# Performance work log

Hardware: AMD Instinct MI355X
Metric: run time of the kernel (lower is better)

The kernel has to match this reference:

```python
import jax, jax.numpy as jnp
import numpy as np

N = 20000    # nodes (spots)
E = 320000   # edges per graph (~16 avg degree)
IN = 256     # input feature dim per omics
H = 128      # hidden dim (n_hidden)
L = 3        # layers_nums


def _sage_gcn(src, dst, x, W, b):
    # DGL SAGEConv 'gcn': h_i = (sum_{j in N(i)} x_j + x_i) / (deg_i + 1); out = h @ W + b
    msg = jax.ops.segment_sum(x[src], dst, num_segments=N)
    deg = jax.ops.segment_sum(jnp.ones((src.shape[0],), x.dtype), dst, num_segments=N)
    h = (msg + x) / (deg[:, None] + 1.0)
    return h @ W + b


def _encoder(src, dst, x, W0, b0, Ws, bs):
    h = _sage_gcn(src, dst, x, W0, b0)
    hs = [h]
    for i in range(L - 1):  # dropout=0, res=True (not 'res_add') -> plain stack
        h = _sage_gcn(src, dst, h, Ws[i], bs[i])
        hs.append(h)
    return jnp.stack(hs)  # [L, N, H]


def _decoder(src, dst, x, W0, b0, Ws, bs):
    h = _sage_gcn(src, dst, x, W0, b0)
    for i in range(L - 1):
        h = _sage_gcn(src, dst, h, Ws[i], bs[i])
    return h


def _combine(hstack, wt):
    # propagation_layer_combination with from_logits=True
    w = jax.nn.softmax(wt)
    return jnp.einsum('l,lnh->nh', w, hstack), w


def _attn(e1, e2, w_omega, u_omega):
    emb = jnp.stack([e1, e2], axis=1)          # [N, 2, H]
    v = jnp.tanh(emb @ w_omega)                # [N, 2, H]
    vu = (v @ u_omega)[..., 0]                 # [N, 2]
    alpha = jax.nn.softmax(vu + 1e-6, axis=-1)
    return jnp.einsum('nmh,nm->nh', emb, alpha), alpha


def setup_inputs():
    key = jax.random.key(0)
    ks = iter(jax.random.split(key, 48))

    def ei():
        return jax.random.randint(next(ks), (E,), 0, N, dtype=jnp.int32)

    def w(shape):
        return jax.random.normal(next(ks), shape, jnp.float32) * 0.05

    d = {}
    for g in ['e1s', 'e1f', 'e2s', 'e2f']:
        d[g + '_src'] = ei()
        d[g + '_dst'] = ei()
    d['feat1'] = jax.random.normal(next(ks), (N, IN), jnp.float32)
    d['feat2'] = jax.random.normal(next(ks), (N, IN), jnp.float32)
    for p in ['enc1', 'enc2']:
        d[p + '_W0'] = w((IN, H)); d[p + '_b0'] = jnp.zeros((H,), jnp.float32)
        d[p + '_W'] = w((L - 1, H, H)); d[p + '_b'] = jnp.zeros((L - 1, H), jnp.float32)
    for p in ['dec1', 'dec2']:
        d[p + '_W0'] = w((H, IN)); d[p + '_b0'] = jnp.zeros((IN,), jnp.float32)
        d[p + '_W'] = w((L - 1, IN, IN)); d[p + '_b'] = jnp.zeros((L - 1, IN), jnp.float32)
    for p in ['att1', 'att2', 'attc']:
        d[p + '_w'] = w((H, H)); d[p + '_u'] = w((H, 1))
    for p in ['wt1', 'wt2', 'wt3', 'wt4']:
        d[p] = jnp.ones((L,), jnp.float32)
    return d


def reference(e1s_src, e1s_dst, e1f_src, e1f_dst, e2s_src, e2s_dst, e2f_src, e2f_dst,
              feat1, feat2,
              enc1_W0, enc1_b0, enc1_W, enc1_b,
              enc2_W0, enc2_b0, enc2_W, enc2_b,
              dec1_W0, dec1_b0, dec1_W, dec1_b,
              dec2_W0, dec2_b0, dec2_W, dec2_b,
              att1_w, att1_u, att2_w, att2_u, attc_w, attc_u,
              wt1, wt2, wt3, wt4):
    enc1 = lambda s, t, x: _encoder(s, t, x, enc1_W0, enc1_b0, enc1_W, enc1_b)
    enc2 = lambda s, t, x: _encoder(s, t, x, enc2_W0, enc2_b0, enc2_W, enc2_b)
    dec1 = lambda s, t, x: _decoder(s, t, x, dec1_W0, dec1_b0, dec1_W, dec1_b)
    dec2 = lambda s, t, x: _decoder(s, t, x, dec2_W0, dec2_b0, dec2_W, dec2_b)

    x_sp1 = enc1(e1s_src, e1s_dst, feat1)
    x_fe1 = enc1(e1f_src, e1f_dst, feat1)
    e_sp1, w_sp1 = _combine(x_sp1, wt1)
    e_fe1, w_fe1 = _combine(x_fe1, wt2)
    emb1, _ = _attn(e_sp1, e_fe1, att1_w, att1_u)

    x_sp2 = enc2(e2s_src, e2s_dst, feat2)
    x_fe2 = enc2(e2f_src, e2f_dst, feat2)
    e_sp2, w_sp2 = _combine(x_sp2, wt3)
    e_fe2, w_fe2 = _combine(x_fe2, wt4)
    emb2, _ = _attn(e_sp2, e_fe2, att2_w, att2_u)

    emb_comb, alph = _attn(emb1, emb2, attc_w, attc_u)
    d1 = dec1(e1s_src, e1s_dst, emb_comb)
    d2 = dec2(e2s_src, e2s_dst, emb_comb)
    cross1 = enc2(e1s_src, e1s_dst, dec2(e1s_src, e1s_dst, emb1))
    cross2 = enc1(e2s_src, e2s_dst, dec1(e2s_src, e2s_dst, emb2))
    wt = jnp.stack([w_sp1, w_fe1, w_sp2, w_fe2])  # [4, L]
    return (emb_comb, wt, d1, d2, emb1, emb2, cross1, cross2, alph)
```

## Files before the change

kernel.cpp:

```cpp
#include <hip/hip_runtime.h>
#include <math.h>

#define NN 20000
#define NE 320000

typedef _Float16 v8h __attribute__((ext_vector_type(8)));
typedef _Float16 v4h __attribute__((ext_vector_type(4)));
typedef _Float16 v2h __attribute__((ext_vector_type(2)));
typedef float v4f __attribute__((ext_vector_type(4)));


__global__ void k_zero_i32(int* __restrict__ p, int n) {
    int i = blockIdx.x * blockDim.x + threadIdx.x;
    if (i < n) p[i] = 0;
}

__global__ void k_count(const int* __restrict__ d0, const int* __restrict__ d1,
                        const int* __restrict__ d2, const int* __restrict__ d3,
                        int* __restrict__ cnt) {
    int i = blockIdx.x * blockDim.x + threadIdx.x;
    int g = i / NE, e = i - g * NE;
    const int* dp = (g == 0) ? d0 : (g == 1) ? d1 : (g == 2) ? d2 : d3;
    atomicAdd(&cnt[g * NN + dp[e]], 1);
}

__global__ void k_scan(const int* __restrict__ cnt, int* __restrict__ off,
                       float* __restrict__ iv) {
    const int g = blockIdx.x;
    const int* c = cnt + g * NN;
    int* o = off + g * (NN + 1);
    float* ivg = iv + g * NN;
    __shared__ int buf[1024];
    const int t = threadIdx.x;
    int carry = 0;
    for (int base = 0; base < NN; base += 1024) {
        int v = (base + t < NN) ? c[base + t] : 0;
        int run = v;
        buf[t] = run;
        __syncthreads();
        for (int s = 1; s < 1024; s <<= 1) {
            int add = (t >= s) ? buf[t - s] : 0;
            __syncthreads();
            run += add;
            buf[t] = run;
            __syncthreads();
        }
        if (base + t < NN) {
            o[base + t] = carry + run - v;
            ivg[base + t] = 1.0f / (float)(v + 1);
        }
        int tot = buf[1023];
        __syncthreads();
        carry += tot;
    }
    if (t == 0) o[NN] = carry;
}

__global__ void k_cursor(const int* __restrict__ off, int* __restrict__ cur) {
    int i = blockIdx.x * blockDim.x + threadIdx.x;
    if (i >= 4 * NN) return;
    int g = i / NN, n = i - g * NN;
    cur[i] = off[g * (NN + 1) + n];
}

__global__ void k_fill(const int* __restrict__ s0, const int* __restrict__ d0,
                       const int* __restrict__ s1, const int* __restrict__ d1,
                       const int* __restrict__ s2, const int* __restrict__ d2,
                       const int* __restrict__ s3, const int* __restrict__ d3,
                       int* __restrict__ cur, int* __restrict__ csr) {
    int i = blockIdx.x * blockDim.x + threadIdx.x;
    int g = i / NE, e = i - g * NE;
    const int* sp = (g == 0) ? s0 : (g == 1) ? s1 : (g == 2) ? s2 : s3;
    const int* dp = (g == 0) ? d0 : (g == 1) ? d1 : (g == 2) ? d2 : d3;
    int dst = dp[e];
    int p = atomicAdd(&cur[g * NN + dst], 1);
    csr[(size_t)g * NE + p] = sp[e];
}


__global__ void k_wt_softmax(const float* __restrict__ a, const float* __restrict__ b,
                             const float* __restrict__ c, const float* __restrict__ d,
                             float* __restrict__ wsm, float* __restrict__ owt) {
    int t = threadIdx.x;
    if (t >= 4) return;
    const float* p = (t == 0) ? a : (t == 1) ? b : (t == 2) ? c : d;
    float x0 = p[0], x1 = p[1], x2 = p[2];
    float m = fmaxf(x0, fmaxf(x1, x2));
    float e0 = expf(x0 - m), e1 = expf(x1 - m), e2 = expf(x2 - m);
    float inv = 1.0f / (e0 + e1 + e2);
    wsm[t * 3 + 0] = e0 * inv; wsm[t * 3 + 1] = e1 * inv; wsm[t * 3 + 2] = e2 * inv;
    owt[t * 3 + 0] = e0 * inv; owt[t * 3 + 1] = e1 * inv; owt[t * 3 + 2] = e2 * inv;
}

__global__ void k_cvt16(const float* __restrict__ in, _Float16* __restrict__ out, int n4) {
    int i = blockIdx.x * blockDim.x + threadIdx.x;
    if (i >= n4) return;
    float4 v = ((const float4*)in)[i];
    v4h o; o[0] = (_Float16)v.x; o[1] = (_Float16)v.y; o[2] = (_Float16)v.z; o[3] = (_Float16)v.w;
    ((v4h*)out)[i] = o;
}


struct PWArgs { const float* s[15]; };

__global__ __launch_bounds__(256) void k_prepW(PWArgs pa, _Float16* __restrict__ dst) {
    const int wK[15]   = {256,128,128,256,128,128, 128,256,256, 128,256,256, 128,128,128};
    const int wN[15]   = {128,128,128,128,128,128, 256,256,256, 256,256,256, 128,128,128};
    const int wOff[15] = {0,32768,49152,65536,98304,114688,
                          131072,163840,229376, 294912,327680,393216,
                          458752,475136,491520};
    int b = blockIdx.x, w = 0, start = 0;
    for (w = 0; w < 15; ++w) {
        int t = (wK[w] / 64) * (wN[w] / 64);
        if (b < start + t) break;
        start += t;
    }
    const int K = wK[w], N = wN[w];
    const int lt = b - start;
    const int nt = N / 64;
    const int k0 = (lt / nt) * 64, n0 = (lt % nt) * 64;
    const float* src = pa.s[w];
    __shared__ float T[64][65];
    const int t = threadIdx.x;
    const int c4 = (t & 15) * 4;
#pragma unroll
    for (int j = 0; j < 4; ++j) {
        int row = (t >> 4) + 16 * j;
        float4 v = *(const float4*)(src + (size_t)(k0 + row) * N + n0 + c4);
        T[row][c4 + 0] = v.x; T[row][c4 + 1] = v.y; T[row][c4 + 2] = v.z; T[row][c4 + 3] = v.w;
    }
    __syncthreads();
#pragma unroll
    for (int j = 0; j < 4; ++j) {
        int r = (t >> 4) + 16 * j;
        v4h o;
#pragma unroll
        for (int i = 0; i < 4; ++i) o[i] = (_Float16)T[c4 + i][r];
        *(v4h*)(dst + wOff[w] + (size_t)(n0 + r) * K + k0 + c4) = o;
    }
}


template<int DIM>
__global__ void k_spmm(const int* __restrict__ off, const int* __restrict__ csr,
                       const float* __restrict__ iv, const _Float16* __restrict__ x,
                       const float* __restrict__ bias,
                       _Float16* __restrict__ o16, float* __restrict__ o32,
                       _Float16* __restrict__ E, const float* __restrict__ wsc, int emode) {
    int wid = (blockIdx.x * blockDim.x + threadIdx.x) >> 6;
    int lane = threadIdx.x & 63;
    if (wid >= NN) return;
    int e0 = off[wid], e1 = off[wid + 1];
    float sc = iv[wid];
    if (DIM == 256) {
        const int c0 = lane * 4;
        v4h s = *(const v4h*)(x + (size_t)wid * 256 + c0);
        float a0 = (float)s[0], a1 = (float)s[1], a2 = (float)s[2], a3 = (float)s[3];
        for (int e = e0; e < e1; ++e) {
            int sidx = csr[e];
            v4h v = *(const v4h*)(x + (size_t)sidx * 256 + c0);
            a0 += (float)v[0]; a1 += (float)v[1]; a2 += (float)v[2]; a3 += (float)v[3];
        }
        a0 *= sc; a1 *= sc; a2 *= sc; a3 *= sc;
        if (bias) { a0 += bias[c0]; a1 += bias[c0 + 1]; a2 += bias[c0 + 2]; a3 += bias[c0 + 3]; }
        if (o16) {
            v4h o; o[0] = (_Float16)a0; o[1] = (_Float16)a1; o[2] = (_Float16)a2; o[3] = (_Float16)a3;
            *(v4h*)(o16 + (size_t)wid * 256 + c0) = o;
        }
        if (o32) {
            float4 o; o.x = a0; o.y = a1; o.z = a2; o.w = a3;
            *(float4*)(o32 + (size_t)wid * 256 + c0) = o;
        }
    } else {
        const int c0 = lane * 2;
        v2h s = *(const v2h*)(x + (size_t)wid * 128 + c0);
        float a0 = (float)s[0], a1 = (float)s[1];
        for (int e = e0; e < e1; ++e) {
            int sidx = csr[e];
            v2h v = *(const v2h*)(x + (size_t)sidx * 128 + c0);
            a0 += (float)v[0]; a1 += (float)v[1];
        }
        a0 *= sc; a1 *= sc;
        if (bias) { a0 += bias[c0]; a1 += bias[c0 + 1]; }
        if (o16) {
            v2h o; o[0] = (_Float16)a0; o[1] = (_Float16)a1;
            *(v2h*)(o16 + (size_t)wid * 128 + c0) = o;
        }
        if (o32) {
            float2 o; o.x = a0; o.y = a1;
            *(float2*)(o32 + (size_t)wid * 128 + c0) = o;
        }
        if (emode) {
            float wv = *wsc;
            _Float16* ep = E + (size_t)wid * 128 + c0;
            if (emode == 1) {
                v2h o; o[0] = (_Float16)(a0 * wv); o[1] = (_Float16)(a1 * wv);
                *(v2h*)ep = o;
            } else {
                v2h old = *(v2h*)ep;
                v2h o; o[0] = (_Float16)((float)old[0] + a0 * wv);
                o[1] = (_Float16)((float)old[1] + a1 * wv);
                *(v2h*)ep = o;
            }
        }
    }
}


template<int K>
__global__ __launch_bounds__(256) void k_gemm(const _Float16* __restrict__ A,
        const _Float16* __restrict__ Wt, const float* __restrict__ bias,
        int Ntot, int act,
        _Float16* __restrict__ C16, float* __restrict__ C32,
        _Float16* __restrict__ E, const float* __restrict__ wsc, int emode) {
    const int wid = threadIdx.x >> 6, l = threadIdx.x & 63;
    const int r0 = (blockIdx.y * 4 + wid) * 32;
    if (r0 >= NN) return;
    const int colbase = blockIdx.x * 128;
    const int lr = l & 15, lg = l >> 4;
    v4f acc[2][8];
#pragma unroll
    for (int m = 0; m < 2; ++m)
#pragma unroll
        for (int n = 0; n < 8; ++n) acc[m][n] = (v4f){0.f, 0.f, 0.f, 0.f};

    const _Float16* Ab = A + (size_t)(r0 + lr) * K + 8 * lg;
    const _Float16* Wb = Wt + (size_t)(colbase + lr) * K + 8 * lg;
    constexpr int KS = K / 32;
#pragma unroll
    for (int k = 0; k < KS; ++k) {
        v8h a0 = *(const v8h*)(Ab + k * 32);
        v8h a1 = *(const v8h*)(Ab + (size_t)16 * K + k * 32);
        v8h b0 = *(const v8h*)(Wb + k * 32);
        v8h b1 = *(const v8h*)(Wb + (size_t)16 * K + k * 32);
        v8h b2 = *(const v8h*)(Wb + (size_t)32 * K + k * 32);
        v8h b3 = *(const v8h*)(Wb + (size_t)48 * K + k * 32);
        v8h b4 = *(const v8h*)(Wb + (size_t)64 * K + k * 32);
        v8h b5 = *(const v8h*)(Wb + (size_t)80 * K + k * 32);
        v8h b6 = *(const v8h*)(Wb + (size_t)96 * K + k * 32);
        v8h b7 = *(const v8h*)(Wb + (size_t)112 * K + k * 32);
        acc[0][0] = __builtin_amdgcn_mfma_f32_16x16x32_f16(a0, b0, acc[0][0], 0, 0, 0);
        acc[0][1] = __builtin_amdgcn_mfma_f32_16x16x32_f16(a0, b1, acc[0][1], 0, 0, 0);
        acc[0][2] = __builtin_amdgcn_mfma_f32_16x16x32_f16(a0, b2, acc[0][2], 0, 0, 0);
        acc[0][3] = __builtin_amdgcn_mfma_f32_16x16x32_f16(a0, b3, acc[0][3], 0, 0, 0);
        acc[0][4] = __builtin_amdgcn_mfma_f32_16x16x32_f16(a0, b4, acc[0][4], 0, 0, 0);
        acc[0][5] = __builtin_amdgcn_mfma_f32_16x16x32_f16(a0, b5, acc[0][5], 0, 0, 0);
        acc[0][6] = __builtin_amdgcn_mfma_f32_16x16x32_f16(a0, b6, acc[0][6], 0, 0, 0);
        acc[0][7] = __builtin_amdgcn_mfma_f32_16x16x32_f16(a0, b7, acc[0][7], 0, 0, 0);
        acc[1][0] = __builtin_amdgcn_mfma_f32_16x16x32_f16(a1, b0, acc[1][0], 0, 0, 0);
        acc[1][1] = __builtin_amdgcn_mfma_f32_16x16x32_f16(a1, b1, acc[1][1], 0, 0, 0);
        acc[1][2] = __builtin_amdgcn_mfma_f32_16x16x32_f16(a1, b2, acc[1][2], 0, 0, 0);
        acc[1][3] = __builtin_amdgcn_mfma_f32_16x16x32_f16(a1, b3, acc[1][3], 0, 0, 0);
        acc[1][4] = __builtin_amdgcn_mfma_f32_16x16x32_f16(a1, b4, acc[1][4], 0, 0, 0);
        acc[1][5] = __builtin_amdgcn_mfma_f32_16x16x32_f16(a1, b5, acc[1][5], 0, 0, 0);
        acc[1][6] = __builtin_amdgcn_mfma_f32_16x16x32_f16(a1, b6, acc[1][6], 0, 0, 0);
        acc[1][7] = __builtin_amdgcn_mfma_f32_16x16x32_f16(a1, b7, acc[1][7], 0, 0, 0);
    }

    const float wv = emode ? *wsc : 0.f;
#pragma unroll
    for (int m = 0; m < 2; ++m) {
#pragma unroll
        for (int n = 0; n < 8; ++n) {
            const int col = colbase + n * 16 + lr;
            const float bv = bias ? bias[col] : 0.f;
#pragma unroll
            for (int i = 0; i < 4; ++i) {
                const int row = r0 + m * 16 + 4 * lg + i;
                float v = acc[m][n][i] + bv;
                if (act) v = tanhf(v);
                if (C32) C32[(size_t)row * Ntot + col] = v;
                if (C16) C16[(size_t)row * Ntot + col] = (_Float16)v;
                if (emode) {
                    _Float16* ep = E + (size_t)row * 128 + col;
                    if (emode == 1) *ep = (_Float16)(v * wv);
                    else *ep = (_Float16)((float)*ep + v * wv);
                }
            }
        }
    }
}


__global__ void k_attn_fin(const _Float16* __restrict__ e1, const _Float16* __restrict__ e2,
                           const _Float16* __restrict__ v1, const _Float16* __restrict__ v2,
                           const float* __restrict__ u, float* __restrict__ emb32,
                           _Float16* __restrict__ emb16, float* __restrict__ alpha) {
    int w = (blockIdx.x * blockDim.x + threadIdx.x) >> 6;
    int lane = threadIdx.x & 63;
    if (w >= NN) return;
    const int c0 = lane * 2;
    float2 uv = *(const float2*)(u + c0);
    v2h a = *(const v2h*)(v1 + (size_t)w * 128 + c0);
    v2h b = *(const v2h*)(v2 + (size_t)w * 128 + c0);
    float d1 = (float)a[0] * uv.x + (float)a[1] * uv.y;
    float d2 = (float)b[0] * uv.x + (float)b[1] * uv.y;
    for (int s = 32; s > 0; s >>= 1) {
        d1 += __shfl_xor(d1, s, 64);
        d2 += __shfl_xor(d2, s, 64);
    }
    d1 += 1e-6f; d2 += 1e-6f;
    float m = fmaxf(d1, d2);
    float p1 = expf(d1 - m), p2 = expf(d2 - m);
    float inv = 1.0f / (p1 + p2);
    float al1 = p1 * inv, al2 = p2 * inv;
    v2h x1 = *(const v2h*)(e1 + (size_t)w * 128 + c0);
    v2h x2 = *(const v2h*)(e2 + (size_t)w * 128 + c0);
    float o0 = al1 * (float)x1[0] + al2 * (float)x2[0];
    float o1 = al1 * (float)x1[1] + al2 * (float)x2[1];
    float2 o; o.x = o0; o.y = o1;
    *(float2*)(emb32 + (size_t)w * 128 + c0) = o;
    v2h oh; oh[0] = (_Float16)o0; oh[1] = (_Float16)o1;
    *(v2h*)(emb16 + (size_t)w * 128 + c0) = oh;
    if (alpha != nullptr && lane == 0) {
        alpha[(size_t)w * 2 + 0] = al1;
        alpha[(size_t)w * 2 + 1] = al2;
    }
}


static inline char* alignup(char* p, size_t a) {
    return (char*)(((uintptr_t)p + a - 1) & ~(uintptr_t)(a - 1));
}

extern "C" void kernel_launch(void* const* d_in, const int* in_sizes, int n_in,
                              void* d_out, int out_size, void* d_ws, size_t ws_size,
                              hipStream_t stream) {
    (void)in_sizes; (void)n_in; (void)out_size; (void)ws_size;
    const int* esrc[4] = {(const int*)d_in[0], (const int*)d_in[2], (const int*)d_in[4], (const int*)d_in[6]};
    const int* edst[4] = {(const int*)d_in[1], (const int*)d_in[3], (const int*)d_in[5], (const int*)d_in[7]};
    const float* feat1 = (const float*)d_in[8];
    const float* feat2 = (const float*)d_in[9];
    const float* enc_W0[2] = {(const float*)d_in[10], (const float*)d_in[14]};
    const float* enc_b0[2] = {(const float*)d_in[11], (const float*)d_in[15]};
    const float* enc_W[2]  = {(const float*)d_in[12], (const float*)d_in[16]};
    const float* enc_b[2]  = {(const float*)d_in[13], (const float*)d_in[17]};
    const float* dec_W0[2] = {(const float*)d_in[18], (const float*)d_in[22]};
    const float* dec_b0[2] = {(const float*)d_in[19], (const float*)d_in[23]};
    const float* dec_W[2]  = {(const float*)d_in[20], (const float*)d_in[24]};
    const float* dec_b[2]  = {(const float*)d_in[21], (const float*)d_in[25]};
    const float* att_w[3]  = {(const float*)d_in[26], (const float*)d_in[28], (const float*)d_in[30]};
    const float* att_u[3]  = {(const float*)d_in[27], (const float*)d_in[29], (const float*)d_in[31]};
    const float* wt[4]     = {(const float*)d_in[32], (const float*)d_in[33], (const float*)d_in[34], (const float*)d_in[35]};

    float* out = (float*)d_out;
    float* O_embc = out;
    float* O_wt   = out + 2560000;
    float* O_d1   = out + 2560012;
    float* O_d2   = out + 7680012;
    float* O_emb1 = out + 12800012;
    float* O_emb2 = out + 15360012;
    float* O_c1   = out + 17920012;
    float* O_c2   = out + 25600012;
    float* O_alph = out + 33280012;

    _Float16* E1 = (_Float16*)O_c1;
    _Float16* E2 = E1 + (size_t)NN * 128;
    _Float16* E3 = E2 + (size_t)NN * 128;
    _Float16* E4 = E3 + (size_t)NN * 128;
    _Float16* V1 = (_Float16*)O_c2;
    _Float16* V2 = V1 + (size_t)NN * 128;
    _Float16* Xe = (_Float16*)O_c1;

    char* wp = (char*)d_ws;
    int* ws_off = (int*)wp;    wp += (size_t)4 * (NN + 1) * sizeof(int); wp = alignup(wp, 64);
    int* ws_csr = (int*)wp;    wp += (size_t)4 * NE * sizeof(int);
    int* ws_cur = (int*)wp;    wp += (size_t)4 * NN * sizeof(int);
    float* ws_iv = (float*)wp; wp += (size_t)4 * NN * sizeof(float);
    float* ws_w  = (float*)wp; wp += 64;
    _Float16* Wt = (_Float16*)wp; wp += (size_t)507904 * 2; wp = alignup(wp, 64);
    _Float16* F1 = (_Float16*)wp; wp += (size_t)NN * 256 * 2;
    _Float16* F2 = (_Float16*)wp; wp += (size_t)NN * 256 * 2;
    _Float16* Abuf = (_Float16*)wp; wp += (size_t)NN * 256 * 2;
    _Float16* Bbuf = (_Float16*)wp; wp += (size_t)NN * 256 * 2;

    _Float16* XB = F1;
    _Float16* embc16 = F1;
    _Float16* emb1_16 = F1 + (size_t)NN * 128;
    _Float16* emb2_16 = F2;

    const int oEnc1W0 = 0, oEnc1W1 = 32768, oEnc1W2 = 49152;
    const int oEnc2W0 = 65536, oEnc2W1 = 98304, oEnc2W2 = 114688;
    const int oDec1W0 = 131072, oDec1W1 = 163840, oDec1W2 = 229376;
    const int oDec2W0 = 294912, oDec2W1 = 327680, oDec2W2 = 393216;
    const int oAtt1 = 458752, oAtt2 = 475136, oAttc = 491520;
    const int oEncW0[2] = {oEnc1W0, oEnc2W0};
    const int oEncW1[2] = {oEnc1W1, oEnc2W1};
    const int oEncW2[2] = {oEnc1W2, oEnc2W2};
    const int oDecW0[2] = {oDec1W0, oDec2W0};
    const int oDecW1[2] = {oDec1W1, oDec2W1};
    const int oDecW2[2] = {oDec1W2, oDec2W2};

    hipLaunchKernelGGL(k_zero_i32, dim3(313), dim3(256), 0, stream, ws_cur, 4 * NN);
    hipLaunchKernelGGL(k_count, dim3(5000), dim3(256), 0, stream,
                       edst[0], edst[1], edst[2], edst[3], ws_cur);
    hipLaunchKernelGGL(k_scan, dim3(4), dim3(1024), 0, stream, ws_cur, ws_off, ws_iv);
    hipLaunchKernelGGL(k_cursor, dim3(313), dim3(256), 0, stream, ws_off, ws_cur);
    hipLaunchKernelGGL(k_fill, dim3(5000), dim3(256), 0, stream,
                       esrc[0], edst[0], esrc[1], edst[1], esrc[2], edst[2], esrc[3], edst[3],
                       ws_cur, ws_csr);
    hipLaunchKernelGGL(k_wt_softmax, dim3(1), dim3(64), 0, stream,
                       wt[0], wt[1], wt[2], wt[3], ws_w, O_wt);

    PWArgs pa;
    pa.s[0] = enc_W0[0]; pa.s[1] = enc_W[0]; pa.s[2] = enc_W[0] + 16384;
    pa.s[3] = enc_W0[1]; pa.s[4] = enc_W[1]; pa.s[5] = enc_W[1] + 16384;
    pa.s[6] = dec_W0[0]; pa.s[7] = dec_W[0]; pa.s[8] = dec_W[0] + 65536;
    pa.s[9] = dec_W0[1]; pa.s[10] = dec_W[1]; pa.s[11] = dec_W[1] + 65536;
    pa.s[12] = att_w[0]; pa.s[13] = att_w[1]; pa.s[14] = att_w[2];
    hipLaunchKernelGGL(k_prepW, dim3(124), dim3(256), 0, stream, pa, Wt);
    hipLaunchKernelGGL(k_cvt16, dim3(5000), dim3(256), 0, stream, feat1, F1, NN * 64);
    hipLaunchKernelGGL(k_cvt16, dim3(5000), dim3(256), 0, stream, feat2, F2, NN * 64);

    auto spmm128 = [&](int g, const _Float16* x, const float* bias, _Float16* o16, float* o32,
                       _Float16* E, const float* wsc, int em) {
        hipLaunchKernelGGL(k_spmm<128>, dim3(5000), dim3(256), 0, stream,
                           ws_off + g * (NN + 1), ws_csr + (size_t)g * NE, ws_iv + g * NN,
                           x, bias, o16, o32, E, wsc, em);
    };
    auto spmm256 = [&](int g, const _Float16* x, _Float16* o16) {
        hipLaunchKernelGGL(k_spmm<256>, dim3(5000), dim3(256), 0, stream,
                           ws_off + g * (NN + 1), ws_csr + (size_t)g * NE, ws_iv + g * NN,
                           x, nullptr, o16, nullptr, nullptr, nullptr, 0);
    };
    auto gemm128 = [&](const _Float16* A, int wtoff, const float* bias, int Ntot, int act,
                       _Float16* C16, float* C32, _Float16* E, const float* wsc, int em) {
        hipLaunchKernelGGL(k_gemm<128>, dim3(Ntot / 128, 157), dim3(256), 0, stream,
                           A, Wt + wtoff, bias, Ntot, act, C16, C32, E, wsc, em);
    };
    auto gemm256 = [&](const _Float16* A, int wtoff, const float* bias, int Ntot, int act,
                       _Float16* C16, float* C32, _Float16* E, const float* wsc, int em) {
        hipLaunchKernelGGL(k_gemm<256>, dim3(Ntot / 128, 157), dim3(256), 0, stream,
                           A, Wt + wtoff, bias, Ntot, act, C16, C32, E, wsc, em);
    };
    auto afin = [&](const _Float16* x1, const _Float16* x2, const _Float16* vv1, const _Float16* vv2,
                    const float* uu, float* eo32, _Float16* eo16, float* al) {
        hipLaunchKernelGGL(k_attn_fin, dim3(5000), dim3(256), 0, stream,
                           x1, x2, vv1, vv2, uu, eo32, eo16, al);
    };

    gemm256(F1, oEnc1W0, nullptr, 128, 0, Abuf, nullptr, nullptr, nullptr, 0);
    {
        struct Run { int g; _Float16* E; int wi; };
        Run runs[2] = {{0, E1, 0}, {1, E2, 1}};
        for (int r = 0; r < 2; ++r) {
            spmm128(runs[r].g, Abuf, enc_b0[0], Bbuf, nullptr, runs[r].E, ws_w + runs[r].wi * 3 + 0, 1);
            spmm128(runs[r].g, Bbuf, nullptr, XB, nullptr, nullptr, nullptr, 0);
            gemm128(XB, oEnc1W1, enc_b[0], 128, 0, Bbuf, nullptr, runs[r].E, ws_w + runs[r].wi * 3 + 1, 2);
            spmm128(runs[r].g, Bbuf, nullptr, XB, nullptr, nullptr, nullptr, 0);
            gemm128(XB, oEnc1W2, enc_b[0] + 128, 128, 0, nullptr, nullptr, runs[r].E, ws_w + runs[r].wi * 3 + 2, 2);
        }
    }
    gemm256(F2, oEnc2W0, nullptr, 128, 0, Abuf, nullptr, nullptr, nullptr, 0);
    {
        struct Run { int g; _Float16* E; int wi; };
        Run runs[2] = {{2, E3, 2}, {3, E4, 3}};
        for (int r = 0; r < 2; ++r) {
            spmm128(runs[r].g, Abuf, enc_b0[1], Bbuf, nullptr, runs[r].E, ws_w + runs[r].wi * 3 + 0, 1);
            spmm128(runs[r].g, Bbuf, nullptr, XB, nullptr, nullptr, nullptr, 0);
            gemm128(XB, oEnc2W1, enc_b[1], 128, 0, Bbuf, nullptr, runs[r].E, ws_w + runs[r].wi * 3 + 1, 2);
            spmm128(runs[r].g, Bbuf, nullptr, XB, nullptr, nullptr, nullptr, 0);
            gemm128(XB, oEnc2W2, enc_b[1] + 128, 128, 0, nullptr, nullptr, runs[r].E, ws_w + runs[r].wi * 3 + 2, 2);
        }
    }

    gemm128(E1, oAtt1, nullptr, 128, 1, V1, nullptr, nullptr, nullptr, 0);
    gemm128(E2, oAtt1, nullptr, 128, 1, V2, nullptr, nullptr, nullptr, 0);
    afin(E1, E2, V1, V2, att_u[0], O_emb1, emb1_16, nullptr);
    gemm128(E3, oAtt2, nullptr, 128, 1, V1, nullptr, nullptr, nullptr, 0);
    gemm128(E4, oAtt2, nullptr, 128, 1, V2, nullptr, nullptr, nullptr, 0);
    afin(E3, E4, V1, V2, att_u[1], O_emb2, emb2_16, nullptr);
    gemm128(emb1_16, oAttc, nullptr, 128, 1, V1, nullptr, nullptr, nullptr, 0);
    gemm128(emb2_16, oAttc, nullptr, 128, 1, V2, nullptr, nullptr, nullptr, 0);
    afin(emb1_16, emb2_16, V1, V2, att_u[2], O_embc, embc16, O_alph);

    spmm128(0, embc16, nullptr, Abuf, nullptr, nullptr, nullptr, 0);
    for (int dsel = 0; dsel < 2; ++dsel) {
        float* od = (dsel == 0) ? O_d1 : O_d2;
        gemm128(Abuf, oDecW0[dsel], dec_b0[dsel], 256, 0, Bbuf, nullptr, nullptr, nullptr, 0);
        spmm256(0, Bbuf, Xe);
        gemm256(Xe, oDecW1[dsel], dec_b[dsel], 256, 0, Bbuf, nullptr, nullptr, nullptr, 0);
        spmm256(0, Bbuf, Xe);
        gemm256(Xe, oDecW2[dsel], dec_b[dsel] + 256, 256, 0, nullptr, od, nullptr, nullptr, 0);
    }

    for (int c = 0; c < 2; ++c) {
        const int g = (c == 0) ? 0 : 2;
        const int dsel = (c == 0) ? 1 : 0;
        const int enc = (c == 0) ? 1 : 0;
        const _Float16* inp = (c == 0) ? emb1_16 : emb2_16;
        float* oc = (c == 0) ? O_c1 : O_c2;
        spmm128(g, inp, nullptr, Abuf, nullptr, nullptr, nullptr, 0);
        gemm128(Abuf, oDecW0[dsel], dec_b0[dsel], 256, 0, Bbuf, nullptr, nullptr, nullptr, 0);
        spmm256(g, Bbuf, Abuf);
        gemm256(Abuf, oDecW1[dsel], dec_b[dsel], 256, 0, Bbuf, nullptr, nullptr, nullptr, 0);
        spmm256(g, Bbuf, Abuf);
        gemm256(Abuf, oDecW2[dsel], dec_b[dsel] + 256, 256, 0, Bbuf, nullptr, nullptr, nullptr, 0);
        gemm256(Bbuf, oEncW0[enc], nullptr, 128, 0, Abuf, nullptr, nullptr, nullptr, 0);
        spmm128(g, Abuf, enc_b0[enc], Bbuf, oc, nullptr, nullptr, 0);
        spmm128(g, Bbuf, nullptr, Abuf, nullptr, nullptr, nullptr, 0);
        gemm128(Abuf, oEncW1[enc], enc_b[enc], 128, 0, Bbuf, oc + 2560000, nullptr, nullptr, 0);
        spmm128(g, Bbuf, nullptr, Abuf, nullptr, nullptr, nullptr, 0);
        gemm128(Abuf, oEncW2[enc], enc_b[enc] + 128, 128, 0, nullptr, oc + 5120000, nullptr, nullptr, 0);
    }
}
```

Baseline: 2.167 ms.

## Fuse neighbor aggregation with GEMM and attention projection with softmax

Replaces the separate SpMM and GEMM launches with a fused kernel. Each block aggregates 32 nodes' neighbor features into shared memory using 8-wide fp16 vector loads, then multiplies by the layer weight with MFMA and applies bias and the layer-combination epilogue. The attention tanh projection, score reduction and softmax combine also become one kernel, and the two feature conversions merge into one launch. This removes intermediate buffer round trips and many launches. The cost is lower occupancy from shared memory use and less parallelism during the GEMM phase.

```diff
diff --git a/kernel.cpp b/kernel.cpp
--- a/kernel.cpp
+++ b/kernel.cpp
@@ -92,12 +92,16 @@
     owt[t * 3 + 0] = e0 * inv; owt[t * 3 + 1] = e1 * inv; owt[t * 3 + 2] = e2 * inv;
 }
 
-__global__ void k_cvt16(const float* __restrict__ in, _Float16* __restrict__ out, int n4) {
+__global__ void k_cvt16(const float* __restrict__ f1, const float* __restrict__ f2,
+                        _Float16* __restrict__ o1, _Float16* __restrict__ o2, int n4) {
     int i = blockIdx.x * blockDim.x + threadIdx.x;
-    if (i >= n4) return;
-    float4 v = ((const float4*)in)[i];
+    if (i >= 2 * n4) return;
+    const float* in = (i < n4) ? f1 : f2;
+    _Float16* out = (i < n4) ? o1 : o2;
+    int j = (i < n4) ? i : i - n4;
+    float4 v = ((const float4*)in)[j];
     v4h o; o[0] = (_Float16)v.x; o[1] = (_Float16)v.y; o[2] = (_Float16)v.z; o[3] = (_Float16)v.w;
-    ((v4h*)out)[i] = o;
+    ((v4h*)out)[j] = o;
 }
 
 
@@ -141,66 +145,119 @@
 }
 
 
-template<int DIM>
-__global__ void k_spmm(const int* __restrict__ off, const int* __restrict__ csr,
-                       const float* __restrict__ iv, const _Float16* __restrict__ x,
-                       const float* __restrict__ bias,
-                       _Float16* __restrict__ o16, float* __restrict__ o32,
-                       _Float16* __restrict__ E, const float* __restrict__ wsc, int emode) {
-    int wid = (blockIdx.x * blockDim.x + threadIdx.x) >> 6;
-    int lane = threadIdx.x & 63;
-    if (wid >= NN) return;
-    int e0 = off[wid], e1 = off[wid + 1];
-    float sc = iv[wid];
-    if (DIM == 256) {
-        const int c0 = lane * 4;
-        v4h s = *(const v4h*)(x + (size_t)wid * 256 + c0);
-        float a0 = (float)s[0], a1 = (float)s[1], a2 = (float)s[2], a3 = (float)s[3];
-        for (int e = e0; e < e1; ++e) {
-            int sidx = csr[e];
-            v4h v = *(const v4h*)(x + (size_t)sidx * 256 + c0);
-            a0 += (float)v[0]; a1 += (float)v[1]; a2 += (float)v[2]; a3 += (float)v[3];
-        }
-        a0 *= sc; a1 *= sc; a2 *= sc; a3 *= sc;
-        if (bias) { a0 += bias[c0]; a1 += bias[c0 + 1]; a2 += bias[c0 + 2]; a3 += bias[c0 + 3]; }
-        if (o16) {
-            v4h o; o[0] = (_Float16)a0; o[1] = (_Float16)a1; o[2] = (_Float16)a2; o[3] = (_Float16)a3;
-            *(v4h*)(o16 + (size_t)wid * 256 + c0) = o;
-        }
-        if (o32) {
-            float4 o; o.x = a0; o.y = a1; o.z = a2; o.w = a3;
-            *(float4*)(o32 + (size_t)wid * 256 + c0) = o;
-        }
-    } else {
-        const int c0 = lane * 2;
-        v2h s = *(const v2h*)(x + (size_t)wid * 128 + c0);
-        float a0 = (float)s[0], a1 = (float)s[1];
-        for (int e = e0; e < e1; ++e) {
-            int sidx = csr[e];
-            v2h v = *(const v2h*)(x + (size_t)sidx * 128 + c0);
-            a0 += (float)v[0]; a1 += (float)v[1];
-        }
-        a0 *= sc; a1 *= sc;
-        if (bias) { a0 += bias[c0]; a1 += bias[c0 + 1]; }
-        if (o16) {
-            v2h o; o[0] = (_Float16)a0; o[1] = (_Float16)a1;
-            *(v2h*)(o16 + (size_t)wid * 128 + c0) = o;
-        }
-        if (o32) {
-            float2 o; o.x = a0; o.y = a1;
-            *(float2*)(o32 + (size_t)wid * 128 + c0) = o;
-        }
-        if (emode) {
-            float wv = *wsc;
-            _Float16* ep = E + (size_t)wid * 128 + c0;
-            if (emode == 1) {
-                v2h o; o[0] = (_Float16)(a0 * wv); o[1] = (_Float16)(a1 * wv);
-                *(v2h*)ep = o;
+template<int K, int NOUT>
+__global__ __launch_bounds__(256) void k_ag(
+        const int* __restrict__ off, const int* __restrict__ csr, const float* __restrict__ iv,
+        const _Float16* __restrict__ x, const _Float16* __restrict__ Wt,
+        const float* __restrict__ bias,
+        _Float16* __restrict__ o16, float* __restrict__ o32,
+        _Float16* __restrict__ E, const float* __restrict__ wsc, int emode) {
+    __shared__ _Float16 As[32][K + 8];
+    const int t = threadIdx.x, w = t >> 6, l = t & 63;
+    const int r0 = blockIdx.x * 32;
+    {
+        constexpr int LPN = (K == 128) ? 16 : 32;
+        constexpr int NPW = 64 / LPN;
+        const int sub = l / LPN, c = l % LPN;
+#pragma unroll
+        for (int r = 0; r < 8 / NPW; ++r) {
+            const int node = r0 + w * 8 + r * NPW + sub;
+            const int e0 = off[node], cnt = off[node + 1] - e0;
+            float a[8];
+            v8h s = *(const v8h*)(x + (size_t)node * K + c * 8);
+#pragma unroll
+            for (int j = 0; j < 8; ++j) a[j] = (float)s[j];
+            for (int e = 0; e < cnt; ++e) {
+                int idx = csr[e0 + e];
+                v8h v = *(const v8h*)(x + (size_t)idx * K + c * 8);
+#pragma unroll
+                for (int j = 0; j < 8; ++j) a[j] += (float)v[j];
+            }
+            const float sc = iv[node];
+#pragma unroll
+            for (int j = 0; j < 8; ++j) a[j] *= sc;
+            if (Wt == nullptr) {
+                if (bias) {
+#pragma unroll
+                    for (int j = 0; j < 8; ++j) a[j] += bias[c * 8 + j];
+                }
+                if (o16) {
+                    v8h o;
+#pragma unroll
+                    for (int j = 0; j < 8; ++j) o[j] = (_Float16)a[j];
+                    *(v8h*)(o16 + (size_t)node * K + c * 8) = o;
+                }
+                if (o32) {
+                    float4 u0, u1;
+                    u0.x = a[0]; u0.y = a[1]; u0.z = a[2]; u0.w = a[3];
+                    u1.x = a[4]; u1.y = a[5]; u1.z = a[6]; u1.w = a[7];
+                    *(float4*)(o32 + (size_t)node * K + c * 8) = u0;
+                    *(float4*)(o32 + (size_t)node * K + c * 8 + 4) = u1;
+                }
+                if (emode) {
+                    const float wv = *wsc;
+                    _Float16* ep = E + (size_t)node * 128 + c * 8;
+                    v8h o;
+                    if (emode == 1) {
+#pragma unroll
+                        for (int j = 0; j < 8; ++j) o[j] = (_Float16)(a[j] * wv);
+                    } else {
+                        v8h old = *(v8h*)ep;
+#pragma unroll
+                        for (int j = 0; j < 8; ++j) o[j] = (_Float16)((float)old[j] + a[j] * wv);
+                    }
+                    *(v8h*)ep = o;
+                }
             } else {
-                v2h old = *(v2h*)ep;
-                v2h o; o[0] = (_Float16)((float)old[0] + a0 * wv);
-                o[1] = (_Float16)((float)old[1] + a1 * wv);
-                *(v2h*)ep = o;
+                v8h o;
+#pragma unroll
+                for (int j = 0; j < 8; ++j) o[j] = (_Float16)a[j];
+                *(v8h*)&As[w * 8 + r * NPW + sub][c * 8] = o;
+            }
+        }
+    }
+    if (Wt == nullptr) return;
+    __syncthreads();
+    const int lr = l & 15, lg = l >> 4;
+    constexpr int NF = NOUT / 64;
+    const int col0 = w * NF * 16;
+    v4f acc[2][NF];
+#pragma unroll
+    for (int m = 0; m < 2; ++m)
+#pragma unroll
+        for (int n = 0; n < NF; ++n) acc[m][n] = (v4f){0.f, 0.f, 0.f, 0.f};
+    const _Float16* Wb = Wt + (size_t)(col0 + lr) * K + 8 * lg;
+#pragma unroll
+    for (int ks = 0; ks < K / 32; ++ks) {
+        v8h a0 = *(const v8h*)&As[lr][ks * 32 + 8 * lg];
+        v8h a1 = *(const v8h*)&As[lr + 16][ks * 32 + 8 * lg];
+        v8h b[NF];
+#pragma unroll
+        for (int n = 0; n < NF; ++n) b[n] = *(const v8h*)(Wb + (size_t)(16 * n) * K + ks * 32);
+#pragma unroll
+        for (int n = 0; n < NF; ++n) {
+            acc[0][n] = __builtin_amdgcn_mfma_f32_16x16x32_f16(a0, b[n], acc[0][n], 0, 0, 0);
+            acc[1][n] = __builtin_amdgcn_mfma_f32_16x16x32_f16(a1, b[n], acc[1][n], 0, 0, 0);
+        }
+    }
+    const float wv = emode ? *wsc : 0.f;
+#pragma unroll
+    for (int m = 0; m < 2; ++m) {
+#pragma unroll
+        for (int n = 0; n < NF; ++n) {
+            const int col = col0 + n * 16 + lr;
+            const float bv = bias ? bias[col] : 0.f;
+#pragma unroll
+            for (int i = 0; i < 4; ++i) {
+                const int row = r0 + m * 16 + 4 * lg + i;
+                float v = acc[m][n][i] + bv;
+                if (o16) o16[(size_t)row * NOUT + col] = (_Float16)v;
+                if (o32) o32[(size_t)row * NOUT + col] = v;
+                if (NOUT == 128 && emode) {
+                    _Float16* ep = E + (size_t)row * 128 + col;
+                    if (emode == 1) *ep = (_Float16)(v * wv);
+                    else *ep = (_Float16)((float)*ep + v * wv);
+                }
             }
         }
     }
@@ -210,9 +267,7 @@
 template<int K>
 __global__ __launch_bounds__(256) void k_gemm(const _Float16* __restrict__ A,
         const _Float16* __restrict__ Wt, const float* __restrict__ bias,
-        int Ntot, int act,
-        _Float16* __restrict__ C16, float* __restrict__ C32,
-        _Float16* __restrict__ E, const float* __restrict__ wsc, int emode) {
+        int Ntot, _Float16* __restrict__ C16, float* __restrict__ C32) {
     const int wid = threadIdx.x >> 6, l = threadIdx.x & 63;
     const int r0 = (blockIdx.y * 4 + wid) * 32;
     if (r0 >= NN) return;
@@ -223,41 +278,19 @@
     for (int m = 0; m < 2; ++m)
 #pragma unroll
         for (int n = 0; n < 8; ++n) acc[m][n] = (v4f){0.f, 0.f, 0.f, 0.f};
-
     const _Float16* Ab = A + (size_t)(r0 + lr) * K + 8 * lg;
     const _Float16* Wb = Wt + (size_t)(colbase + lr) * K + 8 * lg;
-    constexpr int KS = K / 32;
-#pragma unroll
-    for (int k = 0; k < KS; ++k) {
+#pragma unroll
+    for (int k = 0; k < K / 32; ++k) {
         v8h a0 = *(const v8h*)(Ab + k * 32);
         v8h a1 = *(const v8h*)(Ab + (size_t)16 * K + k * 32);
-        v8h b0 = *(const v8h*)(Wb + k * 32);
-        v8h b1 = *(const v8h*)(Wb + (size_t)16 * K + k * 32);
-        v8h b2 = *(const v8h*)(Wb + (size_t)32 * K + k * 32);
-        v8h b3 = *(const v8h*)(Wb + (size_t)48 * K + k * 32);
-        v8h b4 = *(const v8h*)(Wb + (size_t)64 * K + k * 32);
-        v8h b5 = *(const v8h*)(Wb + (size_t)80 * K + k * 32);
-        v8h b6 = *(const v8h*)(Wb + (size_t)96 * K + k * 32);
-        v8h b7 = *(const v8h*)(Wb + (size_t)112 * K + k * 32);
-        acc[0][0] = __builtin_amdgcn_mfma_f32_16x16x32_f16(a0, b0, acc[0][0], 0, 0, 0);
-        acc[0][1] = __builtin_amdgcn_mfma_f32_16x16x32_f16(a0, b1, acc[0][1], 0, 0, 0);
-        acc[0][2] = __builtin_amdgcn_mfma_f32_16x16x32_f16(a0, b2, acc[0][2], 0, 0, 0);
-        acc[0][3] = __builtin_amdgcn_mfma_f32_16x16x32_f16(a0, b3, acc[0][3], 0, 0, 0);
-        acc[0][4] = __builtin_amdgcn_mfma_f32_16x16x32_f16(a0, b4, acc[0][4], 0, 0, 0);
-        acc[0][5] = __builtin_amdgcn_mfma_f32_16x16x32_f16(a0, b5, acc[0][5], 0, 0, 0);
-        acc[0][6] = __builtin_amdgcn_mfma_f32_16x16x32_f16(a0, b6, acc[0][6], 0, 0, 0);
-        acc[0][7] = __builtin_amdgcn_mfma_f32_16x16x32_f16(a0, b7, acc[0][7], 0, 0, 0);
-        acc[1][0] = __builtin_amdgcn_mfma_f32_16x16x32_f16(a1, b0, acc[1][0], 0, 0, 0);
-        acc[1][1] = __builtin_amdgcn_mfma_f32_16x16x32_f16(a1, b1, acc[1][1], 0, 0, 0);
-        acc[1][2] = __builtin_amdgcn_mfma_f32_16x16x32_f16(a1, b2, acc[1][2], 0, 0, 0);
-        acc[1][3] = __builtin_amdgcn_mfma_f32_16x16x32_f16(a1, b3, acc[1][3], 0, 0, 0);
-        acc[1][4] = __builtin_amdgcn_mfma_f32_16x16x32_f16(a1, b4, acc[1][4], 0, 0, 0);
-        acc[1][5] = __builtin_amdgcn_mfma_f32_16x16x32_f16(a1, b5, acc[1][5], 0, 0, 0);
-        acc[1][6] = __builtin_amdgcn_mfma_f32_16x16x32_f16(a1, b6, acc[1][6], 0, 0, 0);
-        acc[1][7] = __builtin_amdgcn_mfma_f32_16x16x32_f16(a1, b7, acc[1][7], 0, 0, 0);
-    }
-
-    const float wv = emode ? *wsc : 0.f;
+#pragma unroll
+        for (int n = 0; n < 8; ++n) {
+            v8h b = *(const v8h*)(Wb + (size_t)(16 * n) * K + k * 32);
+            acc[0][n] = __builtin_amdgcn_mfma_f32_16x16x32_f16(a0, b, acc[0][n], 0, 0, 0);
+            acc[1][n] = __builtin_amdgcn_mfma_f32_16x16x32_f16(a1, b, acc[1][n], 0, 0, 0);
+        }
+    }
 #pragma unroll
     for (int m = 0; m < 2; ++m) {
 #pragma unroll
@@ -268,53 +301,106 @@
             for (int i = 0; i < 4; ++i) {
                 const int row = r0 + m * 16 + 4 * lg + i;
                 float v = acc[m][n][i] + bv;
-                if (act) v = tanhf(v);
+                if (C16) C16[(size_t)row * Ntot + col] = (_Float16)v;
                 if (C32) C32[(size_t)row * Ntot + col] = v;
-                if (C16) C16[(size_t)row * Ntot + col] = (_Float16)v;
-                if (emode) {
-                    _Float16* ep = E + (size_t)row * 128 + col;
-                    if (emode == 1) *ep = (_Float16)(v * wv);
-                    else *ep = (_Float16)((float)*ep + v * wv);
-                }
             }
         }
     }
 }
 
 
-__global__ void k_attn_fin(const _Float16* __restrict__ e1, const _Float16* __restrict__ e2,
-                           const _Float16* __restrict__ v1, const _Float16* __restrict__ v2,
-                           const float* __restrict__ u, float* __restrict__ emb32,
-                           _Float16* __restrict__ emb16, float* __restrict__ alpha) {
-    int w = (blockIdx.x * blockDim.x + threadIdx.x) >> 6;
-    int lane = threadIdx.x & 63;
-    if (w >= NN) return;
-    const int c0 = lane * 2;
-    float2 uv = *(const float2*)(u + c0);
-    v2h a = *(const v2h*)(v1 + (size_t)w * 128 + c0);
-    v2h b = *(const v2h*)(v2 + (size_t)w * 128 + c0);
-    float d1 = (float)a[0] * uv.x + (float)a[1] * uv.y;
-    float d2 = (float)b[0] * uv.x + (float)b[1] * uv.y;
-    for (int s = 32; s > 0; s >>= 1) {
-        d1 += __shfl_xor(d1, s, 64);
-        d2 += __shfl_xor(d2, s, 64);
-    }
-    d1 += 1e-6f; d2 += 1e-6f;
-    float m = fmaxf(d1, d2);
-    float p1 = expf(d1 - m), p2 = expf(d2 - m);
-    float inv = 1.0f / (p1 + p2);
-    float al1 = p1 * inv, al2 = p2 * inv;
-    v2h x1 = *(const v2h*)(e1 + (size_t)w * 128 + c0);
-    v2h x2 = *(const v2h*)(e2 + (size_t)w * 128 + c0);
-    float o0 = al1 * (float)x1[0] + al2 * (float)x2[0];
-    float o1 = al1 * (float)x1[1] + al2 * (float)x2[1];
-    float2 o; o.x = o0; o.y = o1;
-    *(float2*)(emb32 + (size_t)w * 128 + c0) = o;
-    v2h oh; oh[0] = (_Float16)o0; oh[1] = (_Float16)o1;
-    *(v2h*)(emb16 + (size_t)w * 128 + c0) = oh;
-    if (alpha != nullptr && lane == 0) {
-        alpha[(size_t)w * 2 + 0] = al1;
-        alpha[(size_t)w * 2 + 1] = al2;
+__global__ __launch_bounds__(256) void k_attn(
+        const _Float16* __restrict__ e1, const _Float16* __restrict__ e2,
+        const _Float16* __restrict__ Wg, const float* __restrict__ u,
+        float* __restrict__ o32, _Float16* __restrict__ o16, float* __restrict__ alpha) {
+    __shared__ _Float16 Wl[128][136];
+    __shared__ float pvu[2][4][32];
+    __shared__ float als[32][2];
+    const int t = threadIdx.x, w = t >> 6, l = t & 63;
+    const int r0 = blockIdx.x * 32;
+    for (int j = t; j < 2048; j += 256) {
+        int r = j >> 4, c = j & 15;
+        *(v8h*)&Wl[r][c * 8] = *(const v8h*)(Wg + (size_t)r * 128 + c * 8);
+    }
+    __syncthreads();
+    const int lr = l & 15, lg = l >> 4;
+    const int col0 = w * 32;
+    v4f acc1[2][2], acc2[2][2];
+#pragma unroll
+    for (int m = 0; m < 2; ++m)
+#pragma unroll
+        for (int n = 0; n < 2; ++n) { acc1[m][n] = (v4f){0,0,0,0}; acc2[m][n] = (v4f){0,0,0,0}; }
+    const _Float16* A1 = e1 + (size_t)(r0 + lr) * 128 + 8 * lg;
+    const _Float16* A2 = e2 + (size_t)(r0 + lr) * 128 + 8 * lg;
+#pragma unroll
+    for (int ks = 0; ks < 4; ++ks) {
+        v8h a10 = *(const v8h*)(A1 + ks * 32);
+        v8h a11 = *(const v8h*)(A1 + 16 * 128 + ks * 32);
+        v8h a20 = *(const v8h*)(A2 + ks * 32);
+        v8h a21 = *(const v8h*)(A2 + 16 * 128 + ks * 32);
+        v8h b0 = *(const v8h*)&Wl[col0 + lr][ks * 32 + 8 * lg];
+        v8h b1 = *(const v8h*)&Wl[col0 + 16 + lr][ks * 32 + 8 * lg];
+        acc1[0][0] = __builtin_amdgcn_mfma_f32_16x16x32_f16(a10, b0, acc1[0][0], 0, 0, 0);
+        acc1[0][1] = __builtin_amdgcn_mfma_f32_16x16x32_f16(a10, b1, acc1[0][1], 0, 0, 0);
+        acc1[1][0] = __builtin_amdgcn_mfma_f32_16x16x32_f16(a11, b0, acc1[1][0], 0, 0, 0);
+        acc1[1][1] = __builtin_amdgcn_mfma_f32_16x16x32_f16(a11, b1, acc1[1][1], 0, 0, 0);
+        acc2[0][0] = __builtin_amdgcn_mfma_f32_16x16x32_f16(a20, b0, acc2[0][0], 0, 0, 0);
+        acc2[0][1] = __builtin_amdgcn_mfma_f32_16x16x32_f16(a20, b1, acc2[0][1], 0, 0, 0);
+        acc2[1][0] = __builtin_amdgcn_mfma_f32_16x16x32_f16(a21, b0, acc2[1][0], 0, 0, 0);
+        acc2[1][1] = __builtin_amdgcn_mfma_f32_16x16x32_f16(a21, b1, acc2[1][1], 0, 0, 0);
+    }
+    const float uA = u[col0 + lr], uB = u[col0 + 16 + lr];
+#pragma unroll
+    for (int m = 0; m < 2; ++m)
+#pragma unroll
+        for (int i = 0; i < 4; ++i) {
+            float q1 = tanhf(acc1[m][0][i]) * uA + tanhf(acc1[m][1][i]) * uB;
+            float q2 = tanhf(acc2[m][0][i]) * uA + tanhf(acc2[m][1][i]) * uB;
+#pragma unroll
+            for (int s = 1; s < 16; s <<= 1) {
+                q1 += __shfl_xor(q1, s, 64);
+                q2 += __shfl_xor(q2, s, 64);
+            }
+            if (lr == 0) {
+                pvu[0][w][m * 16 + 4 * lg + i] = q1;
+                pvu[1][w][m * 16 + 4 * lg + i] = q2;
+            }
+        }
+    __syncthreads();
+    if (t < 32) {
+        float s1 = pvu[0][0][t] + pvu[0][1][t] + pvu[0][2][t] + pvu[0][3][t];
+        float s2 = pvu[1][0][t] + pvu[1][1][t] + pvu[1][2][t] + pvu[1][3][t];
+        float mx = fmaxf(s1, s2);
+        float q1 = expf(s1 - mx), q2 = expf(s2 - mx);
+        float inv = 1.0f / (q1 + q2);
+        als[t][0] = q1 * inv; als[t][1] = q2 * inv;
+        if (alpha) {
+            alpha[(size_t)(r0 + t) * 2 + 0] = q1 * inv;
+            alpha[(size_t)(r0 + t) * 2 + 1] = q2 * inv;
+        }
+    }
+    __syncthreads();
+    {
+        const int row = t >> 3, c8 = t & 7;
+        const float a1v = als[row][0], a2v = als[row][1];
+#pragma unroll
+        for (int half = 0; half < 2; ++half) {
+            const int cc = c8 + half * 8;
+            v8h x1 = *(const v8h*)(e1 + (size_t)(r0 + row) * 128 + cc * 8);
+            v8h x2 = *(const v8h*)(e2 + (size_t)(r0 + row) * 128 + cc * 8);
+            float o[8];
+#pragma unroll
+            for (int j = 0; j < 8; ++j) o[j] = a1v * (float)x1[j] + a2v * (float)x2[j];
+            float4 u0, u1;
+            u0.x = o[0]; u0.y = o[1]; u0.z = o[2]; u0.w = o[3];
+            u1.x = o[4]; u1.y = o[5]; u1.z = o[6]; u1.w = o[7];
+            *(float4*)(o32 + (size_t)(r0 + row) * 128 + cc * 8) = u0;
+            *(float4*)(o32 + (size_t)(r0 + row) * 128 + cc * 8 + 4) = u1;
+            v8h oh;
+#pragma unroll
+            for (int j = 0; j < 8; ++j) oh[j] = (_Float16)o[j];
+            *(v8h*)(o16 + (size_t)(r0 + row) * 128 + cc * 8) = oh;
+        }
     }
 }
 
@@ -358,9 +444,7 @@
     _Float16* E2 = E1 + (size_t)NN * 128;
     _Float16* E3 = E2 + (size_t)NN * 128;
     _Float16* E4 = E3 + (size_t)NN * 128;
-    _Float16* V1 = (_Float16*)O_c2;
-    _Float16* V2 = V1 + (size_t)NN * 128;
-    _Float16* Xe = (_Float16*)O_c1;
+    _Float16* Xe = (_Float16*)O_c2;
 
     char* wp = (char*)d_ws;
     int* ws_off = (int*)wp;    wp += (size_t)4 * (NN + 1) * sizeof(int); wp = alignup(wp, 64);
@@ -409,79 +493,67 @@
     pa.s[9] = dec_W0[1]; pa.s[10] = dec_W[1]; pa.s[11] = dec_W[1] + 65536;
     pa.s[12] = att_w[0]; pa.s[13] = att_w[1]; pa.s[14] = att_w[2];
     hipLaunchKernelGGL(k_prepW, dim3(124), dim3(256), 0, stream, pa, Wt);
-    hipLaunchKernelGGL(k_cvt16, dim3(5000), dim3(256), 0, stream, feat1, F1, NN * 64);
-    hipLaunchKernelGGL(k_cvt16, dim3(5000), dim3(256), 0, stream, feat2, F2, NN * 64);
-
-    auto spmm128 = [&](int g, const _Float16* x, const float* bias, _Float16* o16, float* o32,
-                       _Float16* E, const float* wsc, int em) {
-        hipLaunchKernelGGL(k_spmm<128>, dim3(5000), dim3(256), 0, stream,
+    hipLaunchKernelGGL(k_cvt16, dim3(10000), dim3(256), 0, stream, feat1, feat2, F1, F2, NN * 64);
+
+    auto ag128 = [&](int g, const _Float16* x, int wtoff, const float* bias,
+                     _Float16* o16, float* o32, _Float16* E, const float* wsc, int em) {
+        hipLaunchKernelGGL((k_ag<128, 128>), dim3(625), dim3(256), 0, stream,
                            ws_off + g * (NN + 1), ws_csr + (size_t)g * NE, ws_iv + g * NN,
-                           x, bias, o16, o32, E, wsc, em);
+                           x, (wtoff >= 0) ? Wt + wtoff : nullptr, bias, o16, o32, E, wsc, em);
     };
-    auto spmm256 = [&](int g, const _Float16* x, _Float16* o16) {
-        hipLaunchKernelGGL(k_spmm<256>, dim3(5000), dim3(256), 0, stream,
+    auto ag128x256 = [&](int g, const _Float16* x, int wtoff, const float* bias, _Float16* o16) {
+        hipLaunchKernelGGL((k_ag<128, 256>), dim3(625), dim3(256), 0, stream,
                            ws_off + g * (NN + 1), ws_csr + (size_t)g * NE, ws_iv + g * NN,
-                           x, nullptr, o16, nullptr, nullptr, nullptr, 0);
+                           x, Wt + wtoff, bias, o16, nullptr, nullptr, nullptr, 0);
     };
-    auto gemm128 = [&](const _Float16* A, int wtoff, const float* bias, int Ntot, int act,
-                       _Float16* C16, float* C32, _Float16* E, const float* wsc, int em) {
-        hipLaunchKernelGGL(k_gemm<128>, dim3(Ntot / 128, 157), dim3(256), 0, stream,
-                           A, Wt + wtoff, bias, Ntot, act, C16, C32, E, wsc, em);
+    auto ag256 = [&](int g, const _Float16* x, int wtoff, const float* bias,
+                     _Float16* o16, float* o32) {
+        hipLaunchKernelGGL((k_ag<256, 256>), dim3(625), dim3(256), 0, stream,
+                           ws_off + g * (NN + 1), ws_csr + (size_t)g * NE, ws_iv + g * NN,
+                           x, Wt + wtoff, bias, o16, o32, nullptr, nullptr, 0);
     };
-    auto gemm256 = [&](const _Float16* A, int wtoff, const float* bias, int Ntot, int act,
-                       _Float16* C16, float* C32, _Float16* E, const float* wsc, int em) {
-        hipLaunchKernelGGL(k_gemm<256>, dim3(Ntot / 128, 157), dim3(256), 0, stream,
-                           A, Wt + wtoff, bias, Ntot, act, C16, C32, E, wsc, em);
+    auto gemm = [&](int K, const _Float16* A, int wtoff, const float* bias, int Ntot,
+                    _Float16* C16, float* C32) {
+        if (K == 128)
+            hipLaunchKernelGGL(k_gemm<128>, dim3(Ntot / 128, 157), dim3(256), 0, stream,
+                               A, Wt + wtoff, bias, Ntot, C16, C32);
+        else
+            hipLaunchKernelGGL(k_gemm<256>, dim3(Ntot / 128, 157), dim3(256), 0, stream,
+                               A, Wt + wtoff, bias, Ntot, C16, C32);
     };
-    auto afin = [&](const _Float16* x1, const _Float16* x2, const _Float16* vv1, const _Float16* vv2,
-                    const float* uu, float* eo32, _Float16* eo16, float* al) {
-        hipLaunchKernelGGL(k_attn_fin, dim3(5000), dim3(256), 0, stream,
-                           x1, x2, vv1, vv2, uu, eo32, eo16, al);
+    auto attn = [&](const _Float16* x1, const _Float16* x2, int wtoff, const float* uu,
+                    float* eo32, _Float16* eo16, float* al) {
+        hipLaunchKernelGGL(k_attn, dim3(625), dim3(256), 0, stream,
+                           x1, x2, Wt + wtoff, uu, eo32, eo16, al);
     };
 
-    gemm256(F1, oEnc1W0, nullptr, 128, 0, Abuf, nullptr, nullptr, nullptr, 0);
-    {
-        struct Run { int g; _Float16* E; int wi; };
-        Run runs[2] = {{0, E1, 0}, {1, E2, 1}};
-        for (int r = 0; r < 2; ++r) {
-            spmm128(runs[r].g, Abuf, enc_b0[0], Bbuf, nullptr, runs[r].E, ws_w + runs[r].wi * 3 + 0, 1);
-            spmm128(runs[r].g, Bbuf, nullptr, XB, nullptr, nullptr, nullptr, 0);
-            gemm128(XB, oEnc1W1, enc_b[0], 128, 0, Bbuf, nullptr, runs[r].E, ws_w + runs[r].wi * 3 + 1, 2);
-            spmm128(runs[r].g, Bbuf, nullptr, XB, nullptr, nullptr, nullptr, 0);
-            gemm128(XB, oEnc1W2, enc_b[0] + 128, 128, 0, nullptr, nullptr, runs[r].E, ws_w + runs[r].wi * 3 + 2, 2);
-        }
-    }
-    gemm256(F2, oEnc2W0, nullptr, 128, 0, Abuf, nullptr, nullptr, nullptr, 0);
-    {
-        struct Run { int g; _Float16* E; int wi; };
-        Run runs[2] = {{2, E3, 2}, {3, E4, 3}};
-        for (int r = 0; r < 2; ++r) {
-            spmm128(runs[r].g, Abuf, enc_b0[1], Bbuf, nullptr, runs[r].E, ws_w + runs[r].wi * 3 + 0, 1);
-            spmm128(runs[r].g, Bbuf, nullptr, XB, nullptr, nullptr, nullptr, 0);
-            gemm128(XB, oEnc2W1, enc_b[1], 128, 0, Bbuf, nullptr, runs[r].E, ws_w + runs[r].wi * 3 + 1, 2);
-            spmm128(runs[r].g, Bbuf, nullptr, XB, nullptr, nullptr, nullptr, 0);
-            gemm128(XB, oEnc2W2, enc_b[1] + 128, 128, 0, nullptr, nullptr, runs[r].E, ws_w + runs[r].wi * 3 + 2, 2);
-        }
-    }
-
-    gemm128(E1, oAtt1, nullptr, 128, 1, V1, nullptr, nullptr, nullptr, 0);
-    gemm128(E2, oAtt1, nullptr, 128, 1, V2, nullptr, nullptr, nullptr, 0);
-    afin(E1, E2, V1, V2, att_u[0], O_emb1, emb1_16, nullptr);
-    gemm128(E3, oAtt2, nullptr, 128, 1, V1, nullptr, nullptr, nullptr, 0);
-    gemm128(E4, oAtt2, nullptr, 128, 1, V2, nullptr, nullptr, nullptr, 0);
-    afin(E3, E4, V1, V2, att_u[1], O_emb2, emb2_16, nullptr);
-    gemm128(emb1_16, oAttc, nullptr, 128, 1, V1, nullptr, nullptr, nullptr, 0);
-    gemm128(emb2_16, oAttc, nullptr, 128, 1, V2, nullptr, nullptr, nullptr, 0);
-    afin(emb1_16, emb2_16, V1, V2, att_u[2], O_embc, embc16, O_alph);
-
-    spmm128(0, embc16, nullptr, Abuf, nullptr, nullptr, nullptr, 0);
+    gemm(256, F1, oEnc1W0, nullptr, 128, Abuf, nullptr);
+    for (int r = 0; r < 2; ++r) {
+        _Float16* Er = (r == 0) ? E1 : E2;
+        const float* w3 = ws_w + r * 3;
+        ag128(r, Abuf, -1, enc_b0[0], Bbuf, nullptr, Er, w3 + 0, 1);
+        ag128(r, Bbuf, oEnc1W1, enc_b[0], XB, nullptr, Er, w3 + 1, 2);
+        ag128(r, XB, oEnc1W2, enc_b[0] + 128, nullptr, nullptr, Er, w3 + 2, 2);
+    }
+    gemm(256, F2, oEnc2W0, nullptr, 128, Abuf, nullptr);
+    for (int r = 0; r < 2; ++r) {
+        _Float16* Er = (r == 0) ? E3 : E4;
+        const float* w3 = ws_w + (2 + r) * 3;
+        ag128(2 + r, Abuf, -1, enc_b0[1], Bbuf, nullptr, Er, w3 + 0, 1);
+        ag128(2 + r, Bbuf, oEnc2W1, enc_b[1], XB, nullptr, Er, w3 + 1, 2);
+        ag128(2 + r, XB, oEnc2W2, enc_b[1] + 128, nullptr, nullptr, Er, w3 + 2, 2);
+    }
+
+    attn(E1, E2, oAtt1, att_u[0], O_emb1, emb1_16, nullptr);
+    attn(E3, E4, oAtt2, att_u[1], O_emb2, emb2_16, nullptr);
+    attn(emb1_16, emb2_16, oAttc, att_u[2], O_embc, embc16, O_alph);
+
+    ag128(0, embc16, -1, nullptr, Abuf, nullptr, nullptr, nullptr, 0);
     for (int dsel = 0; dsel < 2; ++dsel) {
         float* od = (dsel == 0) ? O_d1 : O_d2;
-        gemm128(Abuf, oDecW0[dsel], dec_b0[dsel], 256, 0, Bbuf, nullptr, nullptr, nullptr, 0);
-        spmm256(0, Bbuf, Xe);
-        gemm256(Xe, oDecW1[dsel], dec_b[dsel], 256, 0, Bbuf, nullptr, nullptr, nullptr, 0);
-        spmm256(0, Bbuf, Xe);
-        gemm256(Xe, oDecW2[dsel], dec_b[dsel] + 256, 256, 0, nullptr, od, nullptr, nullptr, 0);
+        gemm(128, Abuf, oDecW0[dsel], dec_b0[dsel], 256, Bbuf, nullptr);
+        ag256(0, Bbuf, oDecW1[dsel], dec_b[dsel], Xe, nullptr);
+        ag256(0, Xe, oDecW2[dsel], dec_b[dsel] + 256, nullptr, od);
     }
 
     for (int c = 0; c < 2; ++c) {
@@ -490,17 +562,12 @@
         const int enc = (c == 0) ? 1 : 0;
         const _Float16* inp = (c == 0) ? emb1_16 : emb2_16;
         float* oc = (c == 0) ? O_c1 : O_c2;
-        spmm128(g, inp, nullptr, Abuf, nullptr, nullptr, nullptr, 0);
-        gemm128(Abuf, oDecW0[dsel], dec_b0[dsel], 256, 0, Bbuf, nullptr, nullptr, nullptr, 0);
-        spmm256(g, Bbuf, Abuf);
-        gemm256(Abuf, oDecW1[dsel], dec_b[dsel], 256, 0, Bbuf, nullptr, nullptr, nullptr, 0);
-        spmm256(g, Bbuf, Abuf);
-        gemm256(Abuf, oDecW2[dsel], dec_b[dsel] + 256, 256, 0, Bbuf, nullptr, nullptr, nullptr, 0);
-        gemm256(Bbuf, oEncW0[enc], nullptr, 128, 0, Abuf, nullptr, nullptr, nullptr, 0);
-        spmm128(g, Abuf, enc_b0[enc], Bbuf, oc, nullptr, nullptr, 0);
-        spmm128(g, Bbuf, nullptr, Abuf, nullptr, nullptr, nullptr, 0);
-        gemm128(Abuf, oEncW1[enc], enc_b[enc], 128, 0, Bbuf, oc + 2560000, nullptr, nullptr, 0);
-        spmm128(g, Bbuf, nullptr, Abuf, nullptr, nullptr, nullptr, 0);
-        gemm128(Abuf, oEncW2[enc], enc_b[enc] + 128, 128, 0, nullptr, oc + 5120000, nullptr, nullptr, 0);
-    }
-}
+        ag128x256(g, inp, oDecW0[dsel], dec_b0[dsel], Bbuf);
+        ag256(g, Bbuf, oDecW1[dsel], dec_b[dsel], Abuf, nullptr);
+        ag256(g, Abuf, oDecW2[dsel], dec_b[dsel] + 256, Bbuf, nullptr);
+        gemm(256, Bbuf, oEncW0[enc], nullptr, 128, Abuf, nullptr);
+        ag128(g, Abuf, -1, enc_b0[enc], Bbuf, oc, nullptr, nullptr, 0);
+        ag128(g, Bbuf, oEncW1[enc], enc_b[enc], Abuf, oc + 2560000, nullptr, nullptr, 0);
+        ag128(g, Abuf, oEncW2[enc], enc_b[enc] + 128, nullptr, oc + 5120000, nullptr, nullptr, 0);
+    }
+}
```

Result: faster. 1.859 ms (-14.2%).
